# Kernel tuning notes

Hardware: AMD Instinct MI355X
Metric: run time of the kernel (lower is better)

Reference implementation:

```python
import jax, jax.numpy as jnp
import numpy as np

EPS = 1e-8  # torch F.cosine_similarity default eps


def _reliability_map(hard, conf, pseudo_feat, num_classes):
    """Per-(batch,class) confidence-weighted centers + per-pixel cosine sim.

    hard:        [b, H, W] int class assignment defining the segments
    conf:        [b, 1, H, W] per-pixel confidence weights
    pseudo_feat: [b, d, H, W] features
    returns      [b, H, W] cosine similarity of each pixel feature to the
                 weighted-mean center of its assigned class.
    """
    b = hard.shape[0]
    onehot = jax.nn.one_hot(hard, num_classes, dtype=pseudo_feat.dtype)  # [b,H,W,c]
    weighted = pseudo_feat * conf                                        # [b,d,H,W]
    # segment-sum of weighted features per class -> [b,c,d]
    sums = jnp.einsum('bhwc,bdhw->bcd', onehot, weighted)
    counts = onehot.sum(axis=(1, 2))                                     # [b,c]
    # (class_feat * class_conf).mean(dim=1) over the n_i member pixels
    centers = sums / jnp.maximum(counts, 1.0)[..., None]                 # [b,c,d]
    # gather each pixel's class center
    cen_px = centers[jnp.arange(b)[:, None, None], hard]                 # [b,H,W,d]
    feat_px = jnp.transpose(pseudo_feat, (0, 2, 3, 1))                   # [b,H,W,d]
    num = jnp.sum(feat_px * cen_px, axis=-1)
    fn = jnp.maximum(jnp.linalg.norm(feat_px, axis=-1), EPS)
    cn = jnp.maximum(jnp.linalg.norm(cen_px, axis=-1), EPS)
    return num / (fn * cn)                                               # [b,H,W]


def _ce_per_pixel(logits, labels):
    # CrossEntropyLoss(reduction='none'), no class weights
    logp = jax.nn.log_softmax(logits, axis=1)                            # [b,c,H,W]
    picked = jnp.take_along_axis(logp, labels[:, None], axis=1)[:, 0]    # [b,H,W]
    return -picked


def reference(pred_main, pred_aux, feat_main, feat_aux):
    c = pred_main.shape[1]
    # --- no_grad block (stop_gradient) ---
    pm = jax.lax.stop_gradient(pred_main)
    pa = jax.lax.stop_gradient(pred_aux)
    fm = jax.lax.stop_gradient(feat_main)
    fa = jax.lax.stop_gradient(feat_aux)

    hard_main = jnp.argmax(pm, axis=1)                                   # [b,H,W]
    hard_aux = jnp.argmax(pa, axis=1)
    conf_main = jnp.max(jax.nn.softmax(pm, axis=1), axis=1, keepdims=True)  # [b,1,H,W]
    conf_aux = jnp.max(jax.nn.softmax(pa, axis=1), axis=1, keepdims=True)

    conf_mask = conf_main >= conf_aux                                    # [b,1,H,W]
    pseudo_label = jnp.where(conf_mask[:, 0], hard_main, hard_aux)       # [b,H,W]
    pseudo_feature = jnp.where(conf_mask, fm, fa)                        # [b,d,H,W]

    rel_main = _reliability_map(hard_main, conf_main, pseudo_feature, c)
    rel_aux = _reliability_map(hard_aux, conf_aux, pseudo_feature, c)
    # --- end no_grad ---

    ce_main = _ce_per_pixel(pred_main, pseudo_label)
    ce_aux = _ce_per_pixel(pred_aux, pseudo_label)

    loss_main = jnp.sum(ce_main * rel_aux) / jnp.sum(rel_aux)
    loss_aux = jnp.sum(ce_aux * rel_main) / jnp.sum(rel_main)
    return loss_main + loss_aux


def setup_inputs() -> dict:
    key = jax.random.key(0)
    k1, k2, k3, k4 = jax.random.split(key, 4)
    b, c, d, H, W = 4, 4, 32, 512, 512
    return {
        'pred_main': jax.random.normal(k1, (b, c, H, W), dtype=jnp.float32),
        'pred_aux': jax.random.normal(k2, (b, c, H, W), dtype=jnp.float32),
        'feat_main': jax.random.normal(k3, (b, d, H, W), dtype=jnp.float32),
        'feat_aux': jax.random.normal(k4, (b, d, H, W), dtype=jnp.float32),
    }
```

## Files before the change

### kernel.cpp

```cpp
#include <hip/hip_runtime.h>
#include <math.h>

#define HW 262144
#define NB 4
#define NC 4
#define ND 32
#define NPIX (NB * HW)
#define NG 262144
#define EPSF 1e-8f

#define OFF_SUMS    0
#define OFF_COUNTS  1024
#define OFF_CENTERS 1056
#define OFF_CNORM   2080
#define OFF_PART    2112
#define HDR_BYTES   9472
#define OFF_REC     HDR_BYTES
#define OFF_CPK     (OFF_REC + 4L * NG)
#define OFF_CEM     (OFF_CPK + 16L * NG)
#define OFF_CEA     (OFF_CEM + 16L * NG)

#define ELEM(v,e) ((e)==0?(v).x:(e)==1?(v).y:(e)==2?(v).z:(v).w)
#define W32(q,i)  ((i)==0?(q).x:(i)==1?(q).y:(i)==2?(q).z:(q).w)

__device__ __forceinline__ float wave_sum64(float v) {
#pragma unroll
  for (int off = 32; off > 0; off >>= 1) v += __shfl_xor(v, off, 64);
  return v;
}
__device__ __forceinline__ unsigned short f2bf(float f) {
  unsigned u = __float_as_uint(f);
  return (unsigned short)((u + 0x7fffu + ((u >> 16) & 1u)) >> 16);
}

__global__ __launch_bounds__(256) void passA2s(
    const float* __restrict__ pm, const float* __restrict__ pa,
    unsigned* __restrict__ recu, uint4* __restrict__ cpk4,
    float4* __restrict__ cem4, float4* __restrict__ cea4) {
  int p4 = blockIdx.x * 256 + threadIdx.x;
  int b = p4 >> 16;
  int px4 = p4 & 0xFFFF;
  const float4* xb = (const float4*)pm + (((long)b * NC) << 16) + px4;
  const float4* yb = (const float4*)pa + (((long)b * NC) << 16) + px4;
  float4 X0 = xb[0], X1 = xb[1 << 16], X2 = xb[2 << 16], X3 = xb[3 << 16];
  float4 Y0 = yb[0], Y1 = yb[1 << 16], Y2 = yb[2 << 16], Y3 = yb[3 << 16];
  float4 cem, cea;
  uint4 cpk;
  unsigned ru = 0;
#pragma unroll
  for (int e = 0; e < 4; ++e) {
    float x0 = ELEM(X0, e), x1 = ELEM(X1, e), x2 = ELEM(X2, e), x3 = ELEM(X3, e);
    float y0 = ELEM(Y0, e), y1 = ELEM(Y1, e), y2 = ELEM(Y2, e), y3 = ELEM(Y3, e);
    int hm = 0; float bm = x0;
    if (x1 > bm) { bm = x1; hm = 1; }
    if (x2 > bm) { bm = x2; hm = 2; }
    if (x3 > bm) { bm = x3; hm = 3; }
    int ha = 0; float ba = y0;
    if (y1 > ba) { ba = y1; ha = 1; }
    if (y2 > ba) { ba = y2; ha = 2; }
    if (y3 > ba) { ba = y3; ha = 3; }
    float sem = expf(x0 - bm) + expf(x1 - bm) + expf(x2 - bm) + expf(x3 - bm);
    float sea = expf(y0 - ba) + expf(y1 - ba) + expf(y2 - ba) + expf(y3 - ba);
    float confm = 1.0f / sem, confa = 1.0f / sea;
    int mk = (confm >= confa) ? 1 : 0;
    int lab = mk ? hm : ha;
    float xl = lab == 0 ? x0 : lab == 1 ? x1 : lab == 2 ? x2 : x3;
    float yl = lab == 0 ? y0 : lab == 1 ? y1 : lab == 2 ? y2 : y3;
    float vem = bm - xl + logf(sem);
    float vea = ba - yl + logf(sea);
    unsigned pk = (unsigned)f2bf(confm) | ((unsigned)f2bf(confa) << 16);
    if (e == 0) { cem.x = vem; cea.x = vea; cpk.x = pk; }
    if (e == 1) { cem.y = vem; cea.y = vea; cpk.y = pk; }
    if (e == 2) { cem.z = vem; cea.z = vea; cpk.z = pk; }
    if (e == 3) { cem.w = vem; cea.w = vea; cpk.w = pk; }
    ru |= (unsigned)(hm | (ha << 2) | (mk << 4)) << (8 * e);
  }
  cem4[p4] = cem; cea4[p4] = cea; cpk4[p4] = cpk; recu[p4] = ru;
}

__global__ __launch_bounds__(256) void countK(const unsigned* __restrict__ recu,
                                              float* __restrict__ counts) {
  int b = blockIdx.y;
  int t = blockIdx.x * 256 + threadIdx.x;
  float c[8];
#pragma unroll
  for (int j = 0; j < 8; ++j) c[j] = 0.f;
#pragma unroll
  for (int k = 0; k < 8; ++k) {
    unsigned ru = recu[(b << 16) + t + k * 8192];
#pragma unroll
    for (int e = 0; e < 4; ++e) {
      unsigned r = (ru >> (8 * e)) & 0xffu;
      int hm = r & 3, ha = (r >> 2) & 3;
      c[0] += hm == 0 ? 1.f : 0.f; c[1] += hm == 1 ? 1.f : 0.f;
      c[2] += hm == 2 ? 1.f : 0.f; c[3] += hm == 3 ? 1.f : 0.f;
      c[4] += ha == 0 ? 1.f : 0.f; c[5] += ha == 1 ? 1.f : 0.f;
      c[6] += ha == 2 ? 1.f : 0.f; c[7] += ha == 3 ? 1.f : 0.f;
    }
  }
  int lane = threadIdx.x & 63;
#pragma unroll
  for (int j = 0; j < 8; ++j) {
    float v = wave_sum64(c[j]);
    if (lane == 0) atomicAdd(&counts[(j >> 2) * 16 + b * 4 + (j & 3)], v);
  }
}

__global__ __launch_bounds__(256, 2) void fusedBsum(
    const float* __restrict__ fm, const float* __restrict__ fa,
    const unsigned* __restrict__ recu, const uint4* __restrict__ cpk4,
    float* __restrict__ sums) {
  __shared__ float lred[4][256];
  int p4 = blockIdx.x * 256 + threadIdx.x;
  int b = blockIdx.x >> 8;
  int px4 = p4 & 0xFFFF;
  int wave = threadIdx.x >> 6, lane = threadIdx.x & 63;

  unsigned ru = recu[p4];
  uint4 ck = cpk4[p4];
  int mk0 = (ru >> 4) & 1, mk1 = (ru >> 12) & 1;
  int mk2 = (ru >> 20) & 1, mk3 = (ru >> 28) & 1;
  float wmw[4][4], waw[4][4];
#pragma unroll
  for (int e = 0; e < 4; ++e) {
    unsigned r = (ru >> (8 * e)) & 0xffu;
    unsigned pk = W32(ck, e);
    int hm = r & 3, ha = (r >> 2) & 3;
    float cm = __uint_as_float(pk << 16);
    float ca = __uint_as_float(pk & 0xffff0000u);
#pragma unroll
    for (int c = 0; c < 4; ++c) {
      wmw[e][c] = (hm == c) ? cm : 0.f;
      waw[e][c] = (ha == c) ? ca : 0.f;
    }
  }

  const float4* fmb = (const float4*)fm + (((long)(b * ND)) << 16) + px4;
  const float4* fab = (const float4*)fa + (((long)(b * ND)) << 16) + px4;

#pragma unroll 2
  for (int d = 0; d < ND; ++d) {
    float4 vm = fmb[(long)d << 16];
    float4 va = fab[(long)d << 16];
    float ps0 = mk0 ? vm.x : va.x;
    float ps1 = mk1 ? vm.y : va.y;
    float ps2 = mk2 ? vm.z : va.z;
    float ps3 = mk3 ? vm.w : va.w;
    float pp[8];
#pragma unroll
    for (int c = 0; c < 4; ++c) {
      pp[c]     = fmaf(wmw[0][c], ps0, fmaf(wmw[1][c], ps1,
                  fmaf(wmw[2][c], ps2, wmw[3][c] * ps3)));
      pp[4 + c] = fmaf(waw[0][c], ps0, fmaf(waw[1][c], ps1,
                  fmaf(waw[2][c], ps2, waw[3][c] * ps3)));
    }
#pragma unroll
    for (int j = 0; j < 8; ++j) {
      float r = wave_sum64(pp[j]);
      if (lane == 0) lred[wave][d * 8 + j] = r;
    }
  }
  __syncthreads();
  {
    int t = threadIdx.x;
    float v = lred[0][t] + lred[1][t] + lred[2][t] + lred[3][t];
    int d = t >> 3, j = t & 7;
    int map = j >> 2, cls = j & 3;
    atomicAdd(&sums[((map * NB + b) * NC + cls) * ND + d], v);
  }
}

__global__ __launch_bounds__(1024) void passC(
    const float* __restrict__ sums, const float* __restrict__ counts,
    float* __restrict__ centers, float* __restrict__ cnorm) {
  int t = threadIdx.x;
  int g = t >> 5;
  float cv = sums[t] / fmaxf(counts[g], 1.f);
  centers[t] = cv;
  float s = cv * cv;
#pragma unroll
  for (int off = 16; off > 0; off >>= 1) s += __shfl_xor(s, off, 32);
  if ((t & 31) == 0) cnorm[g] = fmaxf(sqrtf(s), EPSF);
}

__global__ __launch_bounds__(256) void passDf32(
    const float* __restrict__ fm, const float* __restrict__ fa,
    const unsigned* __restrict__ recu, const float4* __restrict__ cem4,
    const float4* __restrict__ cea4, const float* __restrict__ centers,
    const float* __restrict__ cnorm, float* __restrict__ part) {
  __shared__ float sc[1024];
  __shared__ float scn[32];
  __shared__ float red[4][4];
  for (int i = threadIdx.x; i < 1024; i += 256) {
    int d = i & 31, cls = (i >> 5) & 3, bb = (i >> 7) & 3, mp = i >> 9;
    sc[d * 32 + mp * 16 + bb * 4 + cls] = centers[i];
  }
  if (threadIdx.x < 32) scn[threadIdx.x] = cnorm[threadIdx.x];
  __syncthreads();

  int p4 = blockIdx.x * 256 + threadIdx.x;
  int b = p4 >> 16;
  int px4 = p4 & 0xFFFF;
  unsigned ru = recu[p4];
  int im[4], ia[4], mk[4];
#pragma unroll
  for (int e = 0; e < 4; ++e) {
    unsigned r = (ru >> (8 * e)) & 0xffu;
    im[e] = b * 4 + (r & 3);
    ia[e] = 16 + b * 4 + ((r >> 2) & 3);
    mk[e] = (r >> 4) & 1;
  }
  const float4* fmb = (const float4*)fm + (((long)(b * ND)) << 16) + px4;
  const float4* fab = (const float4*)fa + (((long)(b * ND)) << 16) + px4;
  float4 nm = {0.f, 0.f, 0.f, 0.f}, na = {0.f, 0.f, 0.f, 0.f},
         fn2 = {0.f, 0.f, 0.f, 0.f};
#pragma unroll 16
  for (int d = 0; d < ND; ++d) {
    float4 vm = fmb[(long)d << 16];
    float4 va = fab[(long)d << 16];
#pragma unroll
    for (int e = 0; e < 4; ++e) {
      float ps = mk[e] ? ELEM(vm, e) : ELEM(va, e);
      float cim = sc[d * 32 + im[e]];
      float cia = sc[d * 32 + ia[e]];
      if (e == 0) { nm.x = fmaf(ps, cim, nm.x); na.x = fmaf(ps, cia, na.x); fn2.x = fmaf(ps, ps, fn2.x); }
      if (e == 1) { nm.y = fmaf(ps, cim, nm.y); na.y = fmaf(ps, cia, na.y); fn2.y = fmaf(ps, ps, fn2.y); }
      if (e == 2) { nm.z = fmaf(ps, cim, nm.z); na.z = fmaf(ps, cia, na.z); fn2.z = fmaf(ps, ps, fn2.z); }
      if (e == 3) { nm.w = fmaf(ps, cim, nm.w); na.w = fmaf(ps, cia, na.w); fn2.w = fmaf(ps, ps, fn2.w); }
    }
  }
  float4 cem = cem4[p4], cea = cea4[p4];
  float s0 = 0.f, s1 = 0.f, s2 = 0.f, s3 = 0.f;
#pragma unroll
  for (int e = 0; e < 4; ++e) {
    float fn = fmaxf(sqrtf(ELEM(fn2, e)), EPSF);
    float rm = ELEM(nm, e) / (fn * scn[im[e]]);
    float ra = ELEM(na, e) / (fn * scn[ia[e]]);
    s0 = fmaf(ELEM(cem, e), ra, s0);
    s1 += ra;
    s2 = fmaf(ELEM(cea, e), rm, s2);
    s3 += rm;
  }
  s0 = wave_sum64(s0); s1 = wave_sum64(s1);
  s2 = wave_sum64(s2); s3 = wave_sum64(s3);
  int wave = threadIdx.x >> 6, lane = threadIdx.x & 63;
  if (lane == 0) { red[wave][0] = s0; red[wave][1] = s1; red[wave][2] = s2; red[wave][3] = s3; }
  __syncthreads();
  if (threadIdx.x < 4) {
    float v = red[0][threadIdx.x] + red[1][threadIdx.x] +
              red[2][threadIdx.x] + red[3][threadIdx.x];
    atomicAdd(&part[(blockIdx.x & 63) * 4 + threadIdx.x], v);
  }
}

__global__ __launch_bounds__(64) void passE(const float* __restrict__ part,
                                            float* __restrict__ out) {
  int t = threadIdx.x;
  float a0 = part[t * 4 + 0], a1 = part[t * 4 + 1];
  float a2 = part[t * 4 + 2], a3 = part[t * 4 + 3];
  a0 = wave_sum64(a0); a1 = wave_sum64(a1);
  a2 = wave_sum64(a2); a3 = wave_sum64(a3);
  if (t == 0) out[0] = a0 / a1 + a2 / a3;
}

extern "C" void kernel_launch(void* const* d_in, const int* in_sizes, int n_in,
                              void* d_out, int out_size, void* d_ws, size_t ws_size,
                              hipStream_t stream) {
  const float* pm = (const float*)d_in[0];
  const float* pa = (const float*)d_in[1];
  const float* fm = (const float*)d_in[2];
  const float* fa = (const float*)d_in[3];

  float* wsf = (float*)d_ws;
  float* sums = wsf + OFF_SUMS;
  float* counts = wsf + OFF_COUNTS;
  float* centers = wsf + OFF_CENTERS;
  float* cnorm = wsf + OFF_CNORM;
  float* part = wsf + OFF_PART;
  char* wsb = (char*)d_ws;
  unsigned* recu = (unsigned*)(wsb + OFF_REC);
  uint4* cpk4 = (uint4*)(wsb + OFF_CPK);
  float4* cem4 = (float4*)(wsb + OFF_CEM);
  float4* cea4 = (float4*)(wsb + OFF_CEA);

  hipMemsetAsync(d_ws, 0, HDR_BYTES, stream);
  passA2s<<<1024, 256, 0, stream>>>(pm, pa, recu, cpk4, cem4, cea4);
  countK<<<dim3(32, 4), 256, 0, stream>>>(recu, counts);
  fusedBsum<<<1024, 256, 0, stream>>>(fm, fa, recu, cpk4, sums);
  passC<<<1, 1024, 0, stream>>>(sums, counts, centers, cnorm);
  passDf32<<<1024, 256, 0, stream>>>(fm, fa, recu, cem4, cea4, centers,
                                     cnorm, part);
  passE<<<1, 64, 0, stream>>>(part, (float*)d_out);
}
```

Before: 199.4 us.

## Restructure segment-sum kernel to accumulate per channel over pixel chunks

The segment-sum kernel is rewritten so each wave owns one feature channel and loops over 512 float4 pixel groups, accumulating eight class sums in registers. The old version did a 64-lane shuffle reduction for every channel and class. Now there is one reduction per wave at the end, with per-pixel labels and confidences staged in shared memory. In exchange, the label/confidence records are re-read by each of the 8 channel blocks (from L2 or memory), and the grid grows to 4096 blocks.

```diff
diff --git a/kernel.cpp b/kernel.cpp
--- a/kernel.cpp
+++ b/kernel.cpp
@@ -106,67 +106,67 @@
   }
 }
 
-__global__ __launch_bounds__(256, 2) void fusedBsum(
+__global__ __launch_bounds__(256) void passB3(
     const float* __restrict__ fm, const float* __restrict__ fa,
     const unsigned* __restrict__ recu, const uint4* __restrict__ cpk4,
     float* __restrict__ sums) {
-  __shared__ float lred[4][256];
-  int p4 = blockIdx.x * 256 + threadIdx.x;
-  int b = blockIdx.x >> 8;
-  int px4 = p4 & 0xFFFF;
+  __shared__ unsigned srec[512];
+  __shared__ uint4 sck[512];
+  int chunk = blockIdx.x;
+  int b = blockIdx.y >> 3;
+  int cblk = blockIdx.y & 7;
   int wave = threadIdx.x >> 6, lane = threadIdx.x & 63;
-
-  unsigned ru = recu[p4];
-  uint4 ck = cpk4[p4];
-  int mk0 = (ru >> 4) & 1, mk1 = (ru >> 12) & 1;
-  int mk2 = (ru >> 20) & 1, mk3 = (ru >> 28) & 1;
-  float wmw[4][4], waw[4][4];
-#pragma unroll
-  for (int e = 0; e < 4; ++e) {
-    unsigned r = (ru >> (8 * e)) & 0xffu;
-    unsigned pk = W32(ck, e);
-    int hm = r & 3, ha = (r >> 2) & 3;
-    float cm = __uint_as_float(pk << 16);
-    float ca = __uint_as_float(pk & 0xffff0000u);
-#pragma unroll
-    for (int c = 0; c < 4; ++c) {
-      wmw[e][c] = (hm == c) ? cm : 0.f;
-      waw[e][c] = (ha == c) ? ca : 0.f;
-    }
-  }
-
-  const float4* fmb = (const float4*)fm + (((long)(b * ND)) << 16) + px4;
-  const float4* fab = (const float4*)fa + (((long)(b * ND)) << 16) + px4;
-
-#pragma unroll 2
-  for (int d = 0; d < ND; ++d) {
-    float4 vm = fmb[(long)d << 16];
-    float4 va = fab[(long)d << 16];
-    float ps0 = mk0 ? vm.x : va.x;
-    float ps1 = mk1 ? vm.y : va.y;
-    float ps2 = mk2 ? vm.z : va.z;
-    float ps3 = mk3 ? vm.w : va.w;
-    float pp[8];
-#pragma unroll
-    for (int c = 0; c < 4; ++c) {
-      pp[c]     = fmaf(wmw[0][c], ps0, fmaf(wmw[1][c], ps1,
-                  fmaf(wmw[2][c], ps2, wmw[3][c] * ps3)));
-      pp[4 + c] = fmaf(waw[0][c], ps0, fmaf(waw[1][c], ps1,
-                  fmaf(waw[2][c], ps2, waw[3][c] * ps3)));
-    }
-#pragma unroll
-    for (int j = 0; j < 8; ++j) {
-      float r = wave_sum64(pp[j]);
-      if (lane == 0) lred[wave][d * 8 + j] = r;
-    }
+  int ch = cblk * 4 + wave;
+
+  long gbase = ((long)b << 16) + (long)chunk * 512;
+  for (int i = threadIdx.x; i < 512; i += 256) {
+    srec[i] = recu[gbase + i];
+    sck[i] = cpk4[gbase + i];
   }
   __syncthreads();
-  {
-    int t = threadIdx.x;
-    float v = lred[0][t] + lred[1][t] + lred[2][t] + lred[3][t];
-    int d = t >> 3, j = t & 7;
-    int map = j >> 2, cls = j & 3;
-    atomicAdd(&sums[((map * NB + b) * NC + cls) * ND + d], v);
+
+  const float4* fmp = (const float4*)fm + (((long)(b * ND + ch)) << 16) +
+                      chunk * 512 + lane;
+  const float4* fap = (const float4*)fa + (((long)(b * ND + ch)) << 16) +
+                      chunk * 512 + lane;
+
+  float acc[8];
+#pragma unroll
+  for (int j = 0; j < 8; ++j) acc[j] = 0.f;
+
+#pragma unroll 8
+  for (int it = 0; it < 8; ++it) {
+    float4 vm = fmp[it * 64];
+    float4 va = fap[it * 64];
+    int g = lane + it * 64;
+    unsigned ru = srec[g];
+    uint4 ck = sck[g];
+#pragma unroll
+    for (int e = 0; e < 4; ++e) {
+      unsigned r = (ru >> (8 * e)) & 0xffu;
+      unsigned pk = W32(ck, e);
+      int hm = r & 3, ha = (r >> 2) & 3, mk = (r >> 4) & 1;
+      float cm = __uint_as_float(pk << 16);
+      float ca = __uint_as_float(pk & 0xffff0000u);
+      float p = mk ? ELEM(vm, e) : ELEM(va, e);
+      acc[0] = fmaf(hm == 0 ? cm : 0.f, p, acc[0]);
+      acc[1] = fmaf(hm == 1 ? cm : 0.f, p, acc[1]);
+      acc[2] = fmaf(hm == 2 ? cm : 0.f, p, acc[2]);
+      acc[3] = fmaf(hm == 3 ? cm : 0.f, p, acc[3]);
+      acc[4] = fmaf(ha == 0 ? ca : 0.f, p, acc[4]);
+      acc[5] = fmaf(ha == 1 ? ca : 0.f, p, acc[5]);
+      acc[6] = fmaf(ha == 2 ? ca : 0.f, p, acc[6]);
+      acc[7] = fmaf(ha == 3 ? ca : 0.f, p, acc[7]);
+    }
+  }
+
+#pragma unroll
+  for (int j = 0; j < 8; ++j) {
+    float v = wave_sum64(acc[j]);
+    if (lane == 0) {
+      int map = j >> 2, cls = j & 3;
+      atomicAdd(&sums[((map * NB + b) * NC + cls) * ND + ch], v);
+    }
   }
 }
 
@@ -286,7 +286,7 @@
   hipMemsetAsync(d_ws, 0, HDR_BYTES, stream);
   passA2s<<<1024, 256, 0, stream>>>(pm, pa, recu, cpk4, cem4, cea4);
   countK<<<dim3(32, 4), 256, 0, stream>>>(recu, counts);
-  fusedBsum<<<1024, 256, 0, stream>>>(fm, fa, recu, cpk4, sums);
+  passB3<<<dim3(128, 32), 256, 0, stream>>>(fm, fa, recu, cpk4, sums);
   passC<<<1, 1024, 0, stream>>>(sums, counts, centers, cnorm);
   passDf32<<<1024, 256, 0, stream>>>(fm, fa, recu, cem4, cea4, centers,
                                      cnorm, part);
```

After: 251.6 us. 26.2% more time.
